# Kernel tuning notes

Hardware: AMD Instinct MI355X
Metric: run time of the kernel (lower is better)

Reference implementation:

```python
import jax, jax.numpy as jnp
import numpy as np

DICE_TH = 0.4
CLS_TH = 0.5
LN_EPS = 1e-5


def setup_inputs() -> dict:
    key = jax.random.key(0)
    P, C, NC, K = 200_000, 256, 200, 24  # points, clicks, classes, latent prototypes
    ks = jax.random.split(key, 6)
    # structured masks: each click targets one of K prototype regions so the
    # dice/cls thresholds yield a non-degenerate grouping
    point_proto = jax.random.randint(ks[0], (P,), 0, K)
    proto_vals = jax.random.uniform(ks[1], (P,))
    click_proto = jax.random.randint(ks[2], (C,), 0, K)
    base = (point_proto[:, None] == click_proto[None, :]).astype(jnp.float32)  # [P, C]
    noise = jax.random.uniform(ks[3], (P, C))
    masks_heatmap = base * (0.6 + 0.4 * proto_vals[:, None]) + 0.02 * noise
    class_emb = jax.random.normal(ks[4], (K, NC)) * 3.0
    cls_logits = class_emb[click_proto] + 0.3 * jax.random.normal(ks[5], (C, NC))
    clicks_list = jax.random.randint(ks[0], (C,), 0, NC)  # unused (random_clicks=True)
    return {"masks_heatmap": masks_heatmap, "cls_logits": cls_logits,
            "clicks_list": clicks_list}


def _associate(masks_heatmap, cls_logits):
    """Greedy dice+cls-similarity grouping (random_clicks=True path).
    Returns labels[c] = leader click index of the group containing click c."""
    M = masks_heatmap                      # [P, C]
    C = M.shape[1]
    s = M.sum(0)                           # [C]
    # dice[i, j] = 2 * m_i . m_j / (sum(m_i) + sum(m_j))  (all pairs at once)
    dice = 2.0 * (M.T @ M) / (s[:, None] + s[None, :])
    # F.layer_norm over last dim, no affine
    mu = cls_logits.mean(-1, keepdims=True)
    var = ((cls_logits - mu) ** 2).mean(-1, keepdims=True)
    p = (cls_logits - mu) / jnp.sqrt(var + LN_EPS)
    sim = p @ p.T                          # [C, C]
    cond = (dice > DICE_TH) & (sim > CLS_TH)

    def step(carry, x):
        assigned, labels = carry
        i, row = x
        # skip if i already suppressed; take unsuppressed clicks matching row i
        take = row & (~assigned) & (~assigned[i])
        return (assigned | take, jnp.where(take, i, labels)), None

    init = (jnp.zeros((C,), bool), jnp.full((C,), -1, jnp.int32))
    (assigned, labels), _ = jax.lax.scan(
        step, init, (jnp.arange(C, dtype=jnp.int32), cond))
    return labels


def _merge(labels, masks_heatmap, cls_logits):
    """reduction='max': per-group max over member clicks. Unused group slots
    (non-leader indices) are zero-filled and flagged by group_valid."""
    C = masks_heatmap.shape[1]
    seg = jnp.where(labels >= 0, labels, C)  # route unassigned to dump segment
    counts = jax.ops.segment_sum(jnp.ones((C,), jnp.float32), seg,
                                 num_segments=C + 1)[:C]
    group_valid = counts > 0
    nm = jax.ops.segment_max(masks_heatmap.T, seg, num_segments=C + 1)[:C]  # [C, P]
    nc = jax.ops.segment_max(cls_logits, seg, num_segments=C + 1)[:C]      # [C, NC]
    new_masks = jnp.where(group_valid[:, None], nm, 0.0).T  # [P, C]
    new_cls = jnp.where(group_valid[:, None], nc, 0.0)      # [C, NC]
    return new_masks, new_cls, group_valid


def reference(masks_heatmap, cls_logits, clicks_list):
    labels = _associate(masks_heatmap, cls_logits)
    new_masks, new_cls, group_valid = _merge(labels, masks_heatmap, cls_logits)
    return labels, group_valid, new_masks, new_cls
```

## Files before the change

kernel.cpp:

```cpp
#include <hip/hip_runtime.h>
#include <cstdint>
#include <cstddef>

constexpr int P  = 200000;
constexpr int C  = 256;
constexpr int NC = 200;
#define DICE_TH 0.4f
#define CLS_TH  0.5f
#define LN_EPS  1e-5f

constexpr int KC = 800;
constexpr int NCHUNK = 250;
constexpr int NSTEP = KC / 32;
constexpr int GP_CHUNK = 48 * 1024;

constexpr size_t WS_GP      = 0;
constexpr size_t WS_G       = 49152000;
constexpr size_t WS_S       = WS_G + 262144;
constexpr size_t WS_PROW    = WS_S + 1024;
constexpr size_t WS_PT      = WS_PROW + 204800;
constexpr size_t WS_COND    = WS_PT + 204800;
constexpr size_t WS_MSTART  = WS_COND + 8192;
constexpr size_t WS_MEMBERS = WS_MSTART + 1280;

typedef float floatx16 __attribute__((ext_vector_type(16)));
typedef __bf16 bf16x8 __attribute__((ext_vector_type(8)));
typedef unsigned short ushort8 __attribute__((ext_vector_type(8)));

__device__ __forceinline__ unsigned short f2bf(float f) {
  unsigned u = __builtin_bit_cast(unsigned, f);
  unsigned r = u + 0x7FFFu + ((u >> 16) & 1u);
  return (unsigned short)(r >> 16);
}

constexpr int LDA = 40;

__global__ __launch_bounds__(256, 1) void gram_full_kernel(
    const float* __restrict__ M, float* __restrict__ Gp,
    float* __restrict__ s) {
  __shared__ unsigned short Bls[256 * LDA];

  const int tid = threadIdx.x;
  const int wv = tid >> 6, lane = tid & 63;
  const int k0 = blockIdx.x * KC;
  const int mrow = lane & 31;
  const int kgrp = (lane >> 5) * 8;

  floatx16 acc[12];
#pragma unroll
  for (int t = 0; t < 12; ++t)
#pragma unroll
    for (int r = 0; r < 16; ++r) acc[t][r] = 0.f;
  float ssum = 0.f;

  const float* col0 = M + tid;
  float va[32];
  {
    const size_t kb = (size_t)k0 * 256;
#pragma unroll
    for (int u = 0; u < 32; ++u) va[u] = col0[kb + (size_t)u * 256];
  }

#define FRAG(ROW, KO)                                                \
  __builtin_bit_cast(bf16x8, *reinterpret_cast<const ushort8*>(      \
                                 &Bls[((ROW) + mrow) * LDA + (KO)]))

  for (int step = 0; step < NSTEP; ++step) {
#pragma unroll
    for (int u = 0; u < 32; ++u) ssum += va[u];
#pragma unroll
    for (int q = 0; q < 4; ++q) {
      ushort8 t8;
#pragma unroll
      for (int m = 0; m < 8; ++m) t8[m] = f2bf(va[q * 8 + m]);
      *reinterpret_cast<ushort8*>(&Bls[tid * LDA + q * 8]) = t8;
    }
    __syncthreads();

    if (step + 1 < NSTEP) {
      const size_t kb = (size_t)(k0 + (step + 1) * 32) * 256;
#pragma unroll
      for (int u = 0; u < 32; ++u) va[u] = col0[kb + (size_t)u * 256];
    }

#pragma unroll
    for (int sub = 0; sub < 2; ++sub) {
      const int ko = sub * 16 + kgrp;
      bf16x8 a0 = FRAG(32 * wv, ko);
      bf16x8 a1 = FRAG(128 + 32 * wv, ko);
#pragma unroll
      for (int cb = 0; cb < 4; ++cb) {
        bf16x8 blo = FRAG(32 * cb, ko);
        acc[cb] = __builtin_amdgcn_mfma_f32_32x32x16_bf16(a0, blo, acc[cb],
                                                          0, 0, 0);
      }
#pragma unroll
      for (int cb = 0; cb < 4; ++cb) {
        bf16x8 bhi = FRAG(128 + 32 * cb, ko);
        acc[4 + cb] = __builtin_amdgcn_mfma_f32_32x32x16_bf16(
            a0, bhi, acc[4 + cb], 0, 0, 0);
        acc[8 + cb] = __builtin_amdgcn_mfma_f32_32x32x16_bf16(
            a1, bhi, acc[8 + cb], 0, 0, 0);
      }
    }
    __syncthreads();
  }
#undef FRAG

  float* base = Gp + (size_t)blockIdx.x * GP_CHUNK;
#pragma unroll
  for (int t = 0; t < 12; ++t) {
    float* dst = base + (size_t)(wv * 12 + t) * 1024 + lane * 16;
#pragma unroll
    for (int q = 0; q < 4; ++q) {
      float4 v = make_float4(acc[t][4 * q], acc[t][4 * q + 1],
                             acc[t][4 * q + 2], acc[t][4 * q + 3]);
      *reinterpret_cast<float4*>(dst + 4 * q) = v;
    }
  }
  atomicAdd(&s[tid], ssum);
}

__global__ __launch_bounds__(256) void reduce_g_kernel(
    const float* __restrict__ Gp, float* __restrict__ G) {
  const int e = blockIdx.x * 256 + threadIdx.x;
  const float* p = Gp + e;
  float a[25];
#pragma unroll
  for (int i = 0; i < 25; ++i) a[i] = 0.f;
  for (int ch = 0; ch < NCHUNK; ch += 25) {
#pragma unroll
    for (int i = 0; i < 25; ++i) a[i] += p[(size_t)(ch + i) * GP_CHUNK];
  }
  float sum = 0.f;
#pragma unroll
  for (int i = 0; i < 25; ++i) sum += a[i];

  const int sub = e >> 10;
  const int idx = e & 1023;
  const int lane = idx >> 4;
  const int r = idx & 15;
  const int wv = sub / 12;
  const int t = sub % 12;
  int rowband, colband;
  bool mirror = false;
  if (t < 4) {
    rowband = 32 * wv; colband = 32 * t;
  } else if (t < 8) {
    rowband = 32 * wv; colband = 128 + 32 * (t - 4); mirror = true;
  } else {
    rowband = 128 + 32 * wv; colband = 128 + 32 * (t - 8);
  }
  const int gr = rowband + (r & 3) + 8 * (r >> 2) + 4 * (lane >> 5);
  const int gc = colband + (lane & 31);
  G[(size_t)gr * 256 + gc] = sum;
  if (mirror) G[(size_t)gc * 256 + gr] = sum;
}

__global__ __launch_bounds__(64) void ln_kernel(const float* __restrict__ cls,
                                                float* __restrict__ p_row,
                                                float* __restrict__ pT) {
  const int c = blockIdx.x;
  const int t = threadIdx.x;
  const float* x = cls + (size_t)c * NC;
  float v0 = x[t];
  float v1 = x[t + 64];
  float v2 = (t < 72) ? x[t + 128] : 0.f;

  float sum = v0 + v1 + v2;
#pragma unroll
  for (int o = 32; o > 0; o >>= 1) sum += __shfl_xor(sum, o);
  const float mu = sum / (float)NC;

  float d0 = v0 - mu, d1 = v1 - mu, d2 = (t < 72) ? (v2 - mu) : 0.f;
  float sq = d0 * d0 + d1 * d1 + d2 * d2;
#pragma unroll
  for (int o = 32; o > 0; o >>= 1) sq += __shfl_xor(sq, o);
  const float var = sq / (float)NC;
  const float inv = 1.0f / sqrtf(var + LN_EPS);

  float p0 = d0 * inv, p1 = d1 * inv, p2 = d2 * inv;
  p_row[(size_t)c * NC + t] = p0;
  p_row[(size_t)c * NC + t + 64] = p1;
  pT[(size_t)t * C + c] = p0;
  pT[(size_t)(t + 64) * C + c] = p1;
  if (t < 72) {
    p_row[(size_t)c * NC + t + 128] = p2;
    pT[(size_t)(t + 128) * C + c] = p2;
  }
}

__global__ __launch_bounds__(256) void cond_kernel(
    const float* __restrict__ G, const float* __restrict__ s,
    const float* __restrict__ p_row, const float* __restrict__ pT,
    unsigned long long* __restrict__ condW) {
  __shared__ float pi[NC];
  const int i = blockIdx.x;
  const int j = threadIdx.x;
  if (j < NC) pi[j] = p_row[(size_t)i * NC + j];
  __syncthreads();

  const float si = s[i];
  const float sj = s[j];
  const float g = G[(size_t)i * C + j];
  const float dice = 2.f * g / (si + sj);

  float a0 = 0.f, a1 = 0.f, a2 = 0.f, a3 = 0.f;
#pragma unroll 2
  for (int k = 0; k < NC; k += 4) {
    a0 = fmaf(pi[k + 0], pT[(size_t)(k + 0) * C + j], a0);
    a1 = fmaf(pi[k + 1], pT[(size_t)(k + 1) * C + j], a1);
    a2 = fmaf(pi[k + 2], pT[(size_t)(k + 2) * C + j], a2);
    a3 = fmaf(pi[k + 3], pT[(size_t)(k + 3) * C + j], a3);
  }
  const float acc = (a0 + a1) + (a2 + a3);

  const bool cnd = (dice > DICE_TH) && (acc > CLS_TH);
  unsigned long long m = __ballot(cnd);
  if ((j & 63) == 0) condW[i * 4 + (j >> 6)] = m;
}

__global__ __launch_bounds__(64) void scan_kernel(
    const unsigned long long* __restrict__ condW,
    float* __restrict__ out_labels, float* __restrict__ out_valid,
    int* __restrict__ mstart, int* __restrict__ members) {
  __shared__ unsigned long long cS[C * 4];
  __shared__ int cnt[C];
  __shared__ int ms[C + 1];
  const int t = threadIdx.x;

  for (int idx = t; idx < C * 4; idx += 64) cS[idx] = condW[idx];
  for (int idx = t; idx < C; idx += 64) cnt[idx] = 0;
  __syncthreads();

  unsigned long long asg[4] = {0ull, 0ull, 0ull, 0ull};
  int lab[4] = {-1, -1, -1, -1};

  unsigned long long r0 = cS[0], r1 = cS[1], r2 = cS[2], r3 = cS[3];
  for (int i = 0; i < C; ++i) {
    const int nx = (i + 1 < C) ? (i + 1) * 4 : 0;
    unsigned long long n0 = cS[nx], n1 = cS[nx + 1], n2 = cS[nx + 2],
                       n3 = cS[nx + 3];
    const int w = i >> 6, b = i & 63;
    if (!((asg[w] >> b) & 1ull)) {
      unsigned long long tk;
      tk = r0 & ~asg[0]; asg[0] |= tk; if ((tk >> t) & 1ull) lab[0] = i;
      tk = r1 & ~asg[1]; asg[1] |= tk; if ((tk >> t) & 1ull) lab[1] = i;
      tk = r2 & ~asg[2]; asg[2] |= tk; if ((tk >> t) & 1ull) lab[2] = i;
      tk = r3 & ~asg[3]; asg[3] |= tk; if ((tk >> t) & 1ull) lab[3] = i;
    }
    r0 = n0; r1 = n1; r2 = n2; r3 = n3;
  }

#pragma unroll
  for (int w = 0; w < 4; ++w)
    if (lab[w] >= 0) atomicAdd(&cnt[lab[w]], 1);
  __syncthreads();

  if (t == 0) {
    ms[0] = 0;
    for (int c2 = 0; c2 < C; ++c2) ms[c2 + 1] = ms[c2] + cnt[c2];
  }
  __syncthreads();
  for (int idx = t; idx < C; idx += 64) cnt[idx] = ms[idx];
  __syncthreads();
#pragma unroll
  for (int w = 0; w < 4; ++w) {
    if (lab[w] >= 0) {
      int pos = atomicAdd(&cnt[lab[w]], 1);
      members[pos] = w * 64 + t;
    }
  }
#pragma unroll
  for (int w = 0; w < 4; ++w) {
    const int col = w * 64 + t;
    out_labels[col] = (float)lab[w];
    out_valid[col] = (ms[col + 1] > ms[col]) ? 1.0f : 0.0f;
  }
  for (int idx = t; idx < C + 1; idx += 64) mstart[idx] = ms[idx];
}

__global__ __launch_bounds__(256) void merge_masks_kernel(
    const float* __restrict__ M, const int* __restrict__ mstart,
    const int* __restrict__ members, float* __restrict__ out_masks) {
  __shared__ float rows[16 * 256];
  __shared__ int msS[C + 1];
  __shared__ int memS[C];
  const int tid = threadIdx.x;
  const size_t p0 = (size_t)blockIdx.x * 16;

  msS[tid] = mstart[tid];
  if (tid == 0) msS[C] = mstart[C];
  memS[tid] = members[tid];

  const float4* src = reinterpret_cast<const float4*>(M + p0 * 256);
#pragma unroll
  for (int it = 0; it < 4; ++it)
    reinterpret_cast<float4*>(rows)[it * 256 + tid] = src[it * 256 + tid];
  __syncthreads();

  const int st = msS[tid], en = msS[tid + 1];
  float mx[16];
  if (en > st) {
    const int m0 = memS[st];
#pragma unroll
    for (int r = 0; r < 16; ++r) mx[r] = rows[r * 256 + m0];
    for (int k = st + 1; k < en; ++k) {
      const int mm = memS[k];
#pragma unroll
      for (int r = 0; r < 16; ++r) mx[r] = fmaxf(mx[r], rows[r * 256 + mm]);
    }
  } else {
#pragma unroll
    for (int r = 0; r < 16; ++r) mx[r] = 0.f;
  }
#pragma unroll
  for (int r = 0; r < 16; ++r) out_masks[(p0 + r) * 256 + tid] = mx[r];
}

__global__ __launch_bounds__(256) void merge_cls_kernel(
    const float* __restrict__ cls, const int* __restrict__ mstart,
    const int* __restrict__ members, float* __restrict__ out_cls) {
  __shared__ int se[2];
  const int c = blockIdx.x;
  const int t = threadIdx.x;
  if (t < 2) se[t] = mstart[c + t];
  __syncthreads();
  const int st = se[0], en = se[1];
  if (t < NC) {
    float mx = 0.f;
    if (en > st) {
      mx = cls[(size_t)members[st] * NC + t];
      for (int k = st + 1; k < en; ++k)
        mx = fmaxf(mx, cls[(size_t)members[k] * NC + t]);
    }
    out_cls[(size_t)c * NC + t] = mx;
  }
}

extern "C" void kernel_launch(void* const* d_in, const int* in_sizes, int n_in,
                              void* d_out, int out_size, void* d_ws,
                              size_t ws_size, hipStream_t stream) {
  const float* M = (const float*)d_in[0];
  const float* cls = (const float*)d_in[1];

  float* out = (float*)d_out;
  char* ws = (char*)d_ws;
  float* Gp = (float*)(ws + WS_GP);
  float* G = (float*)(ws + WS_G);
  float* s = (float*)(ws + WS_S);
  float* p_row = (float*)(ws + WS_PROW);
  float* pT = (float*)(ws + WS_PT);
  unsigned long long* condW = (unsigned long long*)(ws + WS_COND);
  int* mstart = (int*)(ws + WS_MSTART);
  int* members = (int*)(ws + WS_MEMBERS);

  float* out_labels = out;
  float* out_valid = out + 256;
  float* out_masks = out + 512;
  float* out_cls = out + 512 + (size_t)P * 256;

  hipMemsetAsync(ws + WS_S, 0, 1024, stream);

  gram_full_kernel<<<NCHUNK, 256, 0, stream>>>(M, Gp, s);
  reduce_g_kernel<<<GP_CHUNK / 1024 * 4, 256, 0, stream>>>(Gp, G);
  ln_kernel<<<C, 64, 0, stream>>>(cls, p_row, pT);
  cond_kernel<<<C, 256, 0, stream>>>(G, s, p_row, pT, condW);
  scan_kernel<<<1, 64, 0, stream>>>(condW, out_labels, out_valid, mstart,
                                    members);
  merge_masks_kernel<<<P / 16, 256, 0, stream>>>(M, mstart, members, out_masks);
  merge_cls_kernel<<<C, 256, 0, stream>>>(cls, mstart, members, out_cls);
}
```

Before: 455.4 us.

## Stage gram inputs via direct global-to-LDS DMA and vectorize merge-mask stores

The gram kernel now uses global_load_lds to copy fp32 rows of M straight into a double-buffered shared tile. Each wave converts to bf16 while building its MFMA fragments, instead of first staging through registers and a bf16 LDS tile. This is meant to overlap the next chunk's load with the current MFMAs and to free VGPRs, at the cost of redundant per-wave fp32-to-bf16 conversion and strided LDS reads that may bank-conflict. The merge-mask kernel issues its global loads earlier and gives each thread a 4x4 tile so it can write float4 stores. The reduce_g launch count is written as a literal that equals the old expression.

```diff
diff --git a/kernel.cpp b/kernel.cpp
--- a/kernel.cpp
+++ b/kernel.cpp
@@ -33,18 +33,22 @@
   return (unsigned short)(r >> 16);
 }
 
-constexpr int LDA = 40;
-
-__global__ __launch_bounds__(256, 1) void gram_full_kernel(
+__device__ __forceinline__ void dma16(const float* gp, float* lp) {
+  __builtin_amdgcn_global_load_lds(
+      (const __attribute__((address_space(1))) unsigned int*)gp,
+      (__attribute__((address_space(3))) unsigned int*)lp, 16, 0, 0);
+}
+
+__global__ __launch_bounds__(256, 1) void gram_dma_kernel(
     const float* __restrict__ M, float* __restrict__ Gp,
     float* __restrict__ s) {
-  __shared__ unsigned short Bls[256 * LDA];
+  __shared__ float S[2][32][256];
 
   const int tid = threadIdx.x;
   const int wv = tid >> 6, lane = tid & 63;
-  const int k0 = blockIdx.x * KC;
   const int mrow = lane & 31;
   const int kgrp = (lane >> 5) * 8;
+  const int k0 = blockIdx.x * KC;
 
   floatx16 acc[12];
 #pragma unroll
@@ -53,59 +57,54 @@
     for (int r = 0; r < 16; ++r) acc[t][r] = 0.f;
   float ssum = 0.f;
 
-  const float* col0 = M + tid;
-  float va[32];
-  {
-    const size_t kb = (size_t)k0 * 256;
-#pragma unroll
-    for (int u = 0; u < 32; ++u) va[u] = col0[kb + (size_t)u * 256];
-  }
-
-#define FRAG(ROW, KO)                                                \
-  __builtin_bit_cast(bf16x8, *reinterpret_cast<const ushort8*>(      \
-                                 &Bls[((ROW) + mrow) * LDA + (KO)]))
+#pragma unroll
+  for (int r = 0; r < 8; ++r) {
+    const int kg = k0 + wv * 8 + r;
+    dma16(M + (size_t)kg * 256 + lane * 4, &S[0][wv * 8 + r][0]);
+  }
+  __syncthreads();
 
   for (int step = 0; step < NSTEP; ++step) {
-#pragma unroll
-    for (int u = 0; u < 32; ++u) ssum += va[u];
-#pragma unroll
-    for (int q = 0; q < 4; ++q) {
-      ushort8 t8;
-#pragma unroll
-      for (int m = 0; m < 8; ++m) t8[m] = f2bf(va[q * 8 + m]);
-      *reinterpret_cast<ushort8*>(&Bls[tid * LDA + q * 8]) = t8;
+    const int cur = step & 1;
+    const int nxt = cur ^ 1;
+
+    if (step + 1 < NSTEP) {
+      const int kb = k0 + (step + 1) * 32;
+#pragma unroll
+      for (int r = 0; r < 8; ++r)
+        dma16(M + (size_t)(kb + wv * 8 + r) * 256 + lane * 4,
+              &S[nxt][wv * 8 + r][0]);
+    }
+
+#pragma unroll
+    for (int kk = 0; kk < 32; ++kk) ssum += S[cur][kk][tid];
+
+#pragma unroll
+    for (int sub = 0; sub < 2; ++sub) {
+      const int kb2 = sub * 16 + kgrp;
+      bf16x8 fr[8];
+#pragma unroll
+      for (int b = 0; b < 8; ++b) {
+        const int col = b * 32 + mrow;
+        ushort8 u;
+#pragma unroll
+        for (int j = 0; j < 8; ++j) u[j] = f2bf(S[cur][kb2 + j][col]);
+        fr[b] = __builtin_bit_cast(bf16x8, u);
+      }
+#pragma unroll
+      for (int cb = 0; cb < 4; ++cb)
+        acc[cb] = __builtin_amdgcn_mfma_f32_32x32x16_bf16(fr[wv], fr[cb],
+                                                          acc[cb], 0, 0, 0);
+#pragma unroll
+      for (int cb = 0; cb < 4; ++cb) {
+        acc[4 + cb] = __builtin_amdgcn_mfma_f32_32x32x16_bf16(
+            fr[wv], fr[4 + cb], acc[4 + cb], 0, 0, 0);
+        acc[8 + cb] = __builtin_amdgcn_mfma_f32_32x32x16_bf16(
+            fr[4 + wv], fr[4 + cb], acc[8 + cb], 0, 0, 0);
+      }
     }
     __syncthreads();
-
-    if (step + 1 < NSTEP) {
-      const size_t kb = (size_t)(k0 + (step + 1) * 32) * 256;
-#pragma unroll
-      for (int u = 0; u < 32; ++u) va[u] = col0[kb + (size_t)u * 256];
-    }
-
-#pragma unroll
-    for (int sub = 0; sub < 2; ++sub) {
-      const int ko = sub * 16 + kgrp;
-      bf16x8 a0 = FRAG(32 * wv, ko);
-      bf16x8 a1 = FRAG(128 + 32 * wv, ko);
-#pragma unroll
-      for (int cb = 0; cb < 4; ++cb) {
-        bf16x8 blo = FRAG(32 * cb, ko);
-        acc[cb] = __builtin_amdgcn_mfma_f32_32x32x16_bf16(a0, blo, acc[cb],
-                                                          0, 0, 0);
-      }
-#pragma unroll
-      for (int cb = 0; cb < 4; ++cb) {
-        bf16x8 bhi = FRAG(128 + 32 * cb, ko);
-        acc[4 + cb] = __builtin_amdgcn_mfma_f32_32x32x16_bf16(
-            a0, bhi, acc[4 + cb], 0, 0, 0);
-        acc[8 + cb] = __builtin_amdgcn_mfma_f32_32x32x16_bf16(
-            a1, bhi, acc[8 + cb], 0, 0, 0);
-      }
-    }
-    __syncthreads();
-  }
-#undef FRAG
+  }
 
   float* base = Gp + (size_t)blockIdx.x * GP_CHUNK;
 #pragma unroll
@@ -289,33 +288,44 @@
   const int tid = threadIdx.x;
   const size_t p0 = (size_t)blockIdx.x * 16;
 
+  const float4* src = reinterpret_cast<const float4*>(M + p0 * 256);
+  float4 v0 = src[0 * 256 + tid];
+  float4 v1 = src[1 * 256 + tid];
+  float4 v2 = src[2 * 256 + tid];
+  float4 v3 = src[3 * 256 + tid];
   msS[tid] = mstart[tid];
   if (tid == 0) msS[C] = mstart[C];
   memS[tid] = members[tid];
-
-  const float4* src = reinterpret_cast<const float4*>(M + p0 * 256);
-#pragma unroll
-  for (int it = 0; it < 4; ++it)
-    reinterpret_cast<float4*>(rows)[it * 256 + tid] = src[it * 256 + tid];
-  __syncthreads();
-
-  const int st = msS[tid], en = msS[tid + 1];
-  float mx[16];
-  if (en > st) {
-    const int m0 = memS[st];
-#pragma unroll
-    for (int r = 0; r < 16; ++r) mx[r] = rows[r * 256 + m0];
-    for (int k = st + 1; k < en; ++k) {
+  reinterpret_cast<float4*>(rows)[0 * 256 + tid] = v0;
+  reinterpret_cast<float4*>(rows)[1 * 256 + tid] = v1;
+  reinterpret_cast<float4*>(rows)[2 * 256 + tid] = v2;
+  reinterpret_cast<float4*>(rows)[3 * 256 + tid] = v3;
+  __syncthreads();
+
+  const int cb = (tid & 63) * 4;
+  const int rb = (tid >> 6) * 4;
+  float mx[4][4];
+#pragma unroll
+  for (int r = 0; r < 4; ++r)
+#pragma unroll
+    for (int cc = 0; cc < 4; ++cc) mx[r][cc] = 0.f;
+
+#pragma unroll
+  for (int cc = 0; cc < 4; ++cc) {
+    const int col = cb + cc;
+    const int st = msS[col], en = msS[col + 1];
+    for (int k = st; k < en; ++k) {
       const int mm = memS[k];
 #pragma unroll
-      for (int r = 0; r < 16; ++r) mx[r] = fmaxf(mx[r], rows[r * 256 + mm]);
-    }
-  } else {
-#pragma unroll
-    for (int r = 0; r < 16; ++r) mx[r] = 0.f;
-  }
-#pragma unroll
-  for (int r = 0; r < 16; ++r) out_masks[(p0 + r) * 256 + tid] = mx[r];
+      for (int r = 0; r < 4; ++r)
+        mx[r][cc] = fmaxf(mx[r][cc], rows[(rb + r) * 256 + mm]);
+    }
+  }
+#pragma unroll
+  for (int r = 0; r < 4; ++r) {
+    float4 v = make_float4(mx[r][0], mx[r][1], mx[r][2], mx[r][3]);
+    *reinterpret_cast<float4*>(&out_masks[(p0 + rb + r) * 256 + cb]) = v;
+  }
 }
 
 __global__ __launch_bounds__(256) void merge_cls_kernel(
@@ -362,8 +372,8 @@
 
   hipMemsetAsync(ws + WS_S, 0, 1024, stream);
 
-  gram_full_kernel<<<NCHUNK, 256, 0, stream>>>(M, Gp, s);
-  reduce_g_kernel<<<GP_CHUNK / 1024 * 4, 256, 0, stream>>>(Gp, G);
+  gram_dma_kernel<<<NCHUNK, 256, 0, stream>>>(M, Gp, s);
+  reduce_g_kernel<<<192, 256, 0, stream>>>(Gp, G);
   ln_kernel<<<C, 64, 0, stream>>>(cls, p_row, pT);
   cond_kernel<<<C, 256, 0, stream>>>(G, s, p_row, pT, condW);
   scan_kernel<<<1, 64, 0, stream>>>(condW, out_labels, out_valid, mstart,
```

Result: slower. 1.035 ms (+127.3%).
